# Kernel optimization log

Measured on AMD Instinct MI355X. Metric: run time of the kernel, lower is better.

The kernel has to match this reference:

```python
import jax, jax.numpy as jnp
import numpy as np

N_NODES = 100000
N_EDGES = 1600000
D_IN = 128
D_HID = 128
N_CLASSES = 8


def setup_inputs() -> dict:
    key = jax.random.key(0)
    ks = jax.random.split(key, 8)
    x = jax.random.normal(ks[0], (N_NODES, D_IN), dtype=jnp.float32)
    edge_index = jax.random.randint(ks[1], (2, N_EDGES), 0, N_NODES, dtype=jnp.int32)
    # Glorot-ish init for weights, zeros for biases (PyG GCNConv default)
    W1 = jax.random.normal(ks[2], (D_IN, D_HID), dtype=jnp.float32) / np.sqrt(D_IN)
    b1 = jnp.zeros((D_HID,), dtype=jnp.float32)
    W2 = jax.random.normal(ks[3], (D_HID, D_HID), dtype=jnp.float32) / np.sqrt(D_HID)
    b2 = jnp.zeros((D_HID,), dtype=jnp.float32)
    Wout = jax.random.normal(ks[4], (D_HID, N_CLASSES), dtype=jnp.float32) / np.sqrt(D_HID)
    bout = jnp.zeros((N_CLASSES,), dtype=jnp.float32)
    return {"x": x, "edge_index": edge_index, "W1": W1, "b1": b1,
            "W2": W2, "b2": b2, "Wout": Wout, "bout": bout}


def _gcn_conv(h, src, dst, norm, W, b, n_nodes):
    # h: [N, d_in]; src/dst: [E+N] (with self-loops); norm: [E+N]
    h = h @ W                                   # [N, d_out]
    msg = h[src] * norm[:, None]                # gather + edge-wise scale
    agg = jax.ops.segment_sum(msg, dst, num_segments=n_nodes)  # scatter-add
    return agg + b


def reference(x, edge_index, W1, b1, W2, b2, Wout, bout):
    n = x.shape[0]
    loops = jnp.arange(n, dtype=edge_index.dtype)
    src = jnp.concatenate([edge_index[0], loops])   # [E+N]
    dst = jnp.concatenate([edge_index[1], loops])   # [E+N]
    # symmetric normalization D^-1/2 (A+I) D^-1/2
    deg = jax.ops.segment_sum(jnp.ones_like(src, dtype=x.dtype), dst, num_segments=n)
    dinv = jnp.where(deg > 0, jax.lax.rsqrt(deg), 0.0)
    norm = dinv[src] * dinv[dst]                    # [E+N]

    h = _gcn_conv(x, src, dst, norm, W1, b1, n)
    h = jax.nn.relu(h)  # dropout is identity in eval mode
    h = _gcn_conv(h, src, dst, norm, W2, b2, n)
    h = jax.nn.relu(h)
    return jax.nn.softmax(h @ Wout + bout, axis=1)  # [N, 8]
```

## Files before the change

### kernel.cpp

```cpp
#include <hip/hip_runtime.h>
#include <hip/hip_fp16.h>

#define NN 100000
#define NE 1600000
#define D 128
#define NC 8
#define NBUCK 391
#define BCAP 6144
#define CHUNK 4096

typedef _Float16 half8 __attribute__((ext_vector_type(8)));
typedef float f32x4 __attribute__((ext_vector_type(4)));

__global__ __launch_bounds__(256) void k_bscatter(const int* __restrict__ src,
                                                  const int* __restrict__ dst,
                                                  int* __restrict__ bcursor,
                                                  int* __restrict__ staged, int E) {
    __shared__ int h[NBUCK];
    __shared__ int cur[NBUCK];
    const int t = threadIdx.x;
    for (int i = t; i < NBUCK; i += 256) h[i] = 0;
    __syncthreads();
    const int base0 = blockIdx.x * CHUNK;
    int4 d4[4], s4[4];
    bool val[4];
#pragma unroll
    for (int i = 0; i < 4; ++i) {
        int e = base0 + i * 1024 + t * 4;
        val[i] = e < E;
        if (val[i]) {
            d4[i] = *(const int4*)&dst[e];
            s4[i] = *(const int4*)&src[e];
            atomicAdd(&h[d4[i].x >> 8], 1);
            atomicAdd(&h[d4[i].y >> 8], 1);
            atomicAdd(&h[d4[i].z >> 8], 1);
            atomicAdd(&h[d4[i].w >> 8], 1);
        }
    }
    __syncthreads();
    for (int i = t; i < NBUCK; i += 256) {
        int c = h[i];
        cur[i] = c ? (i * BCAP + atomicAdd(&bcursor[i], c)) : 0;
    }
    __syncthreads();
#pragma unroll
    for (int i = 0; i < 4; ++i) {
        if (val[i]) {
            int p;
            p = atomicAdd(&cur[d4[i].x >> 8], 1); staged[p] = s4[i].x * 256 + (d4[i].x & 255);
            p = atomicAdd(&cur[d4[i].y >> 8], 1); staged[p] = s4[i].y * 256 + (d4[i].y & 255);
            p = atomicAdd(&cur[d4[i].z >> 8], 1); staged[p] = s4[i].z * 256 + (d4[i].z & 255);
            p = atomicAdd(&cur[d4[i].w >> 8], 1); staged[p] = s4[i].w * 256 + (d4[i].w & 255);
        }
    }
}

__global__ __launch_bounds__(256) void k_bfill(const int* __restrict__ staged,
                                               const int* __restrict__ bcursor,
                                               int* __restrict__ rowstart,
                                               int* __restrict__ cnt,
                                               float* __restrict__ dinv,
                                               int* __restrict__ csr,
                                               const float* __restrict__ W1,
                                               __half* __restrict__ wt1,
                                               const float* __restrict__ W2,
                                               __half* __restrict__ wt2) {
    const int b = blockIdx.x;
    const int t = threadIdx.x;
    if (b >= NBUCK) {
        const float* W = (b - NBUCK) ? W2 : W1;
        __half* wt = (b - NBUCK) ? wt2 : wt1;
        for (int i = t; i < D * D; i += 256) {
            int k = i >> 7, c = i & 127;
            wt[c * D + k] = __float2half(W[i]);
        }
        return;
    }
    const int bs = b * BCAP;
    const int be = bs + bcursor[b];
    __shared__ int lc[256];
    __shared__ int ls[256];
    __shared__ int sd[256];
    lc[t] = 0;
    __syncthreads();
    for (int i = bs + t; i < be; i += 256) {
        atomicAdd(&lc[staged[i] & 255], 1);
    }
    __syncthreads();
    int v = lc[t];
    sd[t] = v;
    __syncthreads();
    for (int off = 1; off < 256; off <<= 1) {
        int y = (t >= off) ? sd[t - off] : 0;
        __syncthreads();
        sd[t] += y;
        __syncthreads();
    }
    int ex = sd[t] - v;
    ls[t] = bs + ex;
    int node = (b << 8) + t;
    if (node < NN) {
        rowstart[node] = bs + ex;
        cnt[node] = v;
        dinv[node] = rsqrtf((float)(v + 1));
    }
    lc[t] = 0;
    __syncthreads();
    for (int i = bs + t; i < be; i += 256) {
        int e = staged[i];
        int li = e & 255;
        int p = atomicAdd(&lc[li], 1);
        csr[ls[li] + p] = e >> 8;
    }
}

template <bool F32IN>
__global__ __launch_bounds__(256) void k_mgemm(const void* __restrict__ Ain,
                                               const __half* __restrict__ wt,
                                               const float* __restrict__ dinv,
                                               __half* __restrict__ hout) {
    const int tid = threadIdx.x;
    const int lane = tid & 63;
    const int wave = tid >> 6;
    const int wr = wave >> 1, wc = wave & 1;
    const int row0 = blockIdx.x * 32 + wr * 16;
    const int arow = row0 + (lane & 15);
    const int kg = lane >> 4;

    half8 afrag[4];
    if constexpr (F32IN) {
        const float* A = (const float*)Ain;
#pragma unroll
        for (int s = 0; s < 4; ++s) {
            const float* p = &A[(size_t)arow * D + s * 32 + kg * 8];
            float4 f0 = *(const float4*)p;
            float4 f1 = *(const float4*)(p + 4);
            half8 a;
            a[0] = (_Float16)f0.x; a[1] = (_Float16)f0.y;
            a[2] = (_Float16)f0.z; a[3] = (_Float16)f0.w;
            a[4] = (_Float16)f1.x; a[5] = (_Float16)f1.y;
            a[6] = (_Float16)f1.z; a[7] = (_Float16)f1.w;
            afrag[s] = a;
        }
    } else {
        const __half* A = (const __half*)Ain;
#pragma unroll
        for (int s = 0; s < 4; ++s)
            afrag[s] = *(const half8*)&A[(size_t)arow * D + s * 32 + kg * 8];
    }

    f32x4 acc[4] = {};
    const int colbase = wc * 64;
#pragma unroll
    for (int c = 0; c < 4; ++c) {
        const int col = colbase + c * 16 + (lane & 15);
#pragma unroll
        for (int s = 0; s < 4; ++s) {
            half8 b = *(const half8*)&wt[col * D + s * 32 + kg * 8];
            acc[c] = __builtin_amdgcn_mfma_f32_16x16x32_f16(afrag[s], b, acc[c], 0, 0, 0);
        }
    }

#pragma unroll
    for (int r = 0; r < 4; ++r) {
        const int row = row0 + kg * 4 + r;
        const float dv = dinv[row];
#pragma unroll
        for (int c = 0; c < 4; ++c) {
            const int col = colbase + c * 16 + (lane & 15);
            hout[(size_t)row * D + col] = __float2half(acc[c][r] * dv);
        }
    }
}

__device__ inline void add8h(float* acc, float4 raw) {
    const __half2* hp = (const __half2*)&raw;
#pragma unroll
    for (int q = 0; q < 4; ++q) {
        float2 f = __half22float2(hp[q]);
        acc[2 * q] += f.x;
        acc[2 * q + 1] += f.y;
    }
}

__global__ __launch_bounds__(256) void k_agg(const __half* __restrict__ hs,
                                             const int* __restrict__ rowstart,
                                             const int* __restrict__ cnt,
                                             const int* __restrict__ csr_src,
                                             const float* __restrict__ dinv,
                                             const float* __restrict__ bias,
                                             __half* __restrict__ hout) {
    const int node = blockIdx.x * 4 + (threadIdx.x >> 6);
    const int lane = threadIdx.x & 63;
    const int g = lane >> 4;
    const int f8 = (lane & 15) << 3;

    float acc[8] = {};
    if (g == 0) add8h(acc, *(const float4*)&hs[(size_t)node * D + f8]);

    const int c = cnt[node];
    const int* __restrict__ cl = csr_src + rowstart[node];

    int t = g;
    while (t < c) {
        float4 v[8];
#pragma unroll
        for (int i = 0; i < 8; ++i) {
            int tt = t + 4 * i;
            if (tt < c) {
                int s = cl[tt];
                v[i] = *(const float4*)&hs[(size_t)s * D + f8];
            }
        }
#pragma unroll
        for (int i = 0; i < 8; ++i) {
            int tt = t + 4 * i;
            if (tt < c) add8h(acc, v[i]);
        }
        t += 32;
    }

#pragma unroll
    for (int q = 0; q < 8; ++q) {
        acc[q] += __shfl_xor(acc[q], 16);
        acc[q] += __shfl_xor(acc[q], 32);
    }

    if (g == 0) {
        const float dv = dinv[node];
        float r[8];
#pragma unroll
        for (int q = 0; q < 8; ++q) r[q] = fmaxf(fmaf(dv, acc[q], bias[f8 + q]), 0.f);
        union { float4 f; __half2 h[4]; } u;
#pragma unroll
        for (int q = 0; q < 4; ++q) u.h[q] = __floats2half2_rn(r[2 * q], r[2 * q + 1]);
        *(float4*)&hout[(size_t)node * D + f8] = u.f;
    }
}

__global__ void k_out(const __half* __restrict__ h, const float* __restrict__ Wout,
                      const float* __restrict__ bout, float* __restrict__ out, int n) {
    __shared__ float ws[D * NC];
    int tid = threadIdx.x;
    for (int i = tid; i < D * NC; i += 256) ws[i] = Wout[i];
    __syncthreads();
    int node = blockIdx.x * 32 + (tid >> 3);
    int c = tid & 7;
    if (node >= n) return;
    float acc = bout[c];
    const __half* hrow = &h[(size_t)node * D];
#pragma unroll
    for (int k8 = 0; k8 < 16; ++k8) {
        float4 raw = *(const float4*)&hrow[k8 * 8];
        const __half2* hp = (const __half2*)&raw;
#pragma unroll
        for (int q = 0; q < 4; ++q) {
            float2 f = __half22float2(hp[q]);
            int k = k8 * 8 + 2 * q;
            acc += f.x * ws[k * NC + c] + f.y * ws[(k + 1) * NC + c];
        }
    }
    float m = acc;
#pragma unroll
    for (int off = 1; off < 8; off <<= 1) m = fmaxf(m, __shfl_xor(m, off));
    float e = __expf(acc - m);
    float ssum = e;
#pragma unroll
    for (int off = 1; off < 8; off <<= 1) ssum += __shfl_xor(ssum, off);
    out[(size_t)node * NC + c] = e / ssum;
}

extern "C" void kernel_launch(void* const* d_in, const int* in_sizes, int n_in,
                              void* d_out, int out_size, void* d_ws, size_t ws_size,
                              hipStream_t stream) {
    const float* x    = (const float*)d_in[0];
    const int*   ei   = (const int*)d_in[1];
    const float* W1   = (const float*)d_in[2];
    const float* b1   = (const float*)d_in[3];
    const float* W2   = (const float*)d_in[4];
    const float* b2   = (const float*)d_in[5];
    const float* Wout = (const float*)d_in[6];
    const float* bout = (const float*)d_in[7];
    float* out = (float*)d_out;

    size_t off = 0;
    char* base = (char*)d_ws;
    auto alloc = [&](size_t bytes) -> void* {
        void* p = base + off;
        off += (bytes + 255) & ~(size_t)255;
        return p;
    };
    int*    cnt      = (int*)alloc((size_t)NN * 4);
    int*    rowstart = (int*)alloc((size_t)NN * 4);
    int*    bcursor  = (int*)alloc((size_t)(NBUCK + 1) * 4);
    int*    csr      = (int*)alloc((size_t)NBUCK * BCAP * 4);
    float*  dinv     = (float*)alloc((size_t)NN * 4);
    __half* wt1      = (__half*)alloc((size_t)D * D * 2);
    __half* wt2      = (__half*)alloc((size_t)D * D * 2);
    __half* h16a     = (__half*)alloc((size_t)NN * D * 2);
    __half* h16f     = (__half*)alloc((size_t)NN * D * 2);
    __half* h16b     = (__half*)alloc((size_t)NN * D * 2);
    int*    staged   = (int*)alloc((size_t)NBUCK * BCAP * 4);
    if (off > ws_size) return;

    const int* src = ei;
    const int* dst = ei + NE;

    int bin_grid = (NE + CHUNK - 1) / CHUNK;
    hipMemsetAsync(bcursor, 0, (size_t)NBUCK * 4, stream);
    k_bscatter<<<bin_grid, 256, 0, stream>>>(src, dst, bcursor, staged, NE);
    k_bfill<<<NBUCK + 2, 256, 0, stream>>>(staged, bcursor, rowstart, cnt, dinv, csr,
                                           W1, wt1, W2, wt2);

    int gemm_grid = NN / 32;
    int agg_grid = NN / 4;
    k_mgemm<true><<<gemm_grid, 256, 0, stream>>>(x, wt1, dinv, h16a);
    k_agg<<<agg_grid, 256, 0, stream>>>(h16a, rowstart, cnt, csr, dinv, b1, h16f);
    k_mgemm<false><<<gemm_grid, 256, 0, stream>>>(h16f, wt2, dinv, h16a);
    k_agg<<<agg_grid, 256, 0, stream>>>(h16a, rowstart, cnt, csr, dinv, b2, h16b);
    k_out<<<(NN + 31) / 32, 256, 0, stream>>>(h16b, Wout, bout, out, NN);
}
```

Before: 267.1 us.

## Compute degrees with global atomics and co-schedule bucket scatter with first GEMM

Degree counts now come from a separate pass that uses global atomics on dst, so dinv can be recomputed inline from cnt and the dinv buffer is dropped. The bucket-scatter blocks and the first-layer GEMM blocks are merged into one launch, letting the edge binning overlap the dense GEMM. The scatter chunk size is raised to four times the edge count per block. The cost is an extra pass over dst with contended global atomics, plus re-reading dst in the scatter instead of keeping it in registers.

Result: slower. 325.1 us (+21.7%).

```diff
diff --git a/kernel.cpp b/kernel.cpp
--- a/kernel.cpp
+++ b/kernel.cpp
@@ -7,123 +7,48 @@
 #define NC 8
 #define NBUCK 391
 #define BCAP 6144
-#define CHUNK 4096
+#define CHUNK 16384
+#define NBLK_SC ((NE + CHUNK - 1) / CHUNK)
 
 typedef _Float16 half8 __attribute__((ext_vector_type(8)));
 typedef float f32x4 __attribute__((ext_vector_type(4)));
 
-__global__ __launch_bounds__(256) void k_bscatter(const int* __restrict__ src,
-                                                  const int* __restrict__ dst,
-                                                  int* __restrict__ bcursor,
-                                                  int* __restrict__ staged, int E) {
-    __shared__ int h[NBUCK];
-    __shared__ int cur[NBUCK];
+__global__ __launch_bounds__(256) void k_prep(const float* __restrict__ W1,
+                                              __half* __restrict__ wt1,
+                                              const float* __restrict__ W2,
+                                              __half* __restrict__ wt2,
+                                              const int* __restrict__ dst,
+                                              int* __restrict__ cnt, int E) {
     const int t = threadIdx.x;
-    for (int i = t; i < NBUCK; i += 256) h[i] = 0;
-    __syncthreads();
-    const int base0 = blockIdx.x * CHUNK;
-    int4 d4[4], s4[4];
-    bool val[4];
-#pragma unroll
-    for (int i = 0; i < 4; ++i) {
-        int e = base0 + i * 1024 + t * 4;
-        val[i] = e < E;
-        if (val[i]) {
-            d4[i] = *(const int4*)&dst[e];
-            s4[i] = *(const int4*)&src[e];
-            atomicAdd(&h[d4[i].x >> 8], 1);
-            atomicAdd(&h[d4[i].y >> 8], 1);
-            atomicAdd(&h[d4[i].z >> 8], 1);
-            atomicAdd(&h[d4[i].w >> 8], 1);
-        }
-    }
-    __syncthreads();
-    for (int i = t; i < NBUCK; i += 256) {
-        int c = h[i];
-        cur[i] = c ? (i * BCAP + atomicAdd(&bcursor[i], c)) : 0;
-    }
-    __syncthreads();
-#pragma unroll
-    for (int i = 0; i < 4; ++i) {
-        if (val[i]) {
-            int p;
-            p = atomicAdd(&cur[d4[i].x >> 8], 1); staged[p] = s4[i].x * 256 + (d4[i].x & 255);
-            p = atomicAdd(&cur[d4[i].y >> 8], 1); staged[p] = s4[i].y * 256 + (d4[i].y & 255);
-            p = atomicAdd(&cur[d4[i].z >> 8], 1); staged[p] = s4[i].z * 256 + (d4[i].z & 255);
-            p = atomicAdd(&cur[d4[i].w >> 8], 1); staged[p] = s4[i].w * 256 + (d4[i].w & 255);
-        }
-    }
-}
-
-__global__ __launch_bounds__(256) void k_bfill(const int* __restrict__ staged,
-                                               const int* __restrict__ bcursor,
-                                               int* __restrict__ rowstart,
-                                               int* __restrict__ cnt,
-                                               float* __restrict__ dinv,
-                                               int* __restrict__ csr,
-                                               const float* __restrict__ W1,
-                                               __half* __restrict__ wt1,
-                                               const float* __restrict__ W2,
-                                               __half* __restrict__ wt2) {
-    const int b = blockIdx.x;
-    const int t = threadIdx.x;
-    if (b >= NBUCK) {
-        const float* W = (b - NBUCK) ? W2 : W1;
-        __half* wt = (b - NBUCK) ? wt2 : wt1;
+    if (blockIdx.x < 2) {
+        const float* W = blockIdx.x ? W2 : W1;
+        __half* wt = blockIdx.x ? wt2 : wt1;
         for (int i = t; i < D * D; i += 256) {
             int k = i >> 7, c = i & 127;
             wt[c * D + k] = __float2half(W[i]);
         }
         return;
     }
-    const int bs = b * BCAP;
-    const int be = bs + bcursor[b];
-    __shared__ int lc[256];
-    __shared__ int ls[256];
-    __shared__ int sd[256];
-    lc[t] = 0;
-    __syncthreads();
-    for (int i = bs + t; i < be; i += 256) {
-        atomicAdd(&lc[staged[i] & 255], 1);
-    }
-    __syncthreads();
-    int v = lc[t];
-    sd[t] = v;
-    __syncthreads();
-    for (int off = 1; off < 256; off <<= 1) {
-        int y = (t >= off) ? sd[t - off] : 0;
-        __syncthreads();
-        sd[t] += y;
-        __syncthreads();
-    }
-    int ex = sd[t] - v;
-    ls[t] = bs + ex;
-    int node = (b << 8) + t;
-    if (node < NN) {
-        rowstart[node] = bs + ex;
-        cnt[node] = v;
-        dinv[node] = rsqrtf((float)(v + 1));
-    }
-    lc[t] = 0;
-    __syncthreads();
-    for (int i = bs + t; i < be; i += 256) {
-        int e = staged[i];
-        int li = e & 255;
-        int p = atomicAdd(&lc[li], 1);
-        csr[ls[li] + p] = e >> 8;
+    int e0 = (blockIdx.x - 2) * 1024 + t * 4;
+    if (e0 < E) {
+        int4 d4 = *(const int4*)&dst[e0];
+        atomicAdd(&cnt[d4.x], 1);
+        atomicAdd(&cnt[d4.y], 1);
+        atomicAdd(&cnt[d4.z], 1);
+        atomicAdd(&cnt[d4.w], 1);
     }
 }
 
 template <bool F32IN>
-__global__ __launch_bounds__(256) void k_mgemm(const void* __restrict__ Ain,
-                                               const __half* __restrict__ wt,
-                                               const float* __restrict__ dinv,
-                                               __half* __restrict__ hout) {
+__device__ __forceinline__ void gemm_body(const void* __restrict__ Ain,
+                                          const __half* __restrict__ wt,
+                                          const int* __restrict__ cnt,
+                                          __half* __restrict__ hout, int gb) {
     const int tid = threadIdx.x;
     const int lane = tid & 63;
     const int wave = tid >> 6;
     const int wr = wave >> 1, wc = wave & 1;
-    const int row0 = blockIdx.x * 32 + wr * 16;
+    const int row0 = gb * 32 + wr * 16;
     const int arow = row0 + (lane & 15);
     const int kg = lane >> 4;
 
@@ -164,13 +89,105 @@
 #pragma unroll
     for (int r = 0; r < 4; ++r) {
         const int row = row0 + kg * 4 + r;
-        const float dv = dinv[row];
+        const float dv = rsqrtf((float)(cnt[row] + 1));
 #pragma unroll
         for (int c = 0; c < 4; ++c) {
             const int col = colbase + c * 16 + (lane & 15);
             hout[(size_t)row * D + col] = __float2half(acc[c][r] * dv);
         }
     }
+}
+
+__global__ __launch_bounds__(256) void k_work(const int* __restrict__ src,
+                                              const int* __restrict__ dst,
+                                              int* __restrict__ bcursor,
+                                              int* __restrict__ staged,
+                                              const float* __restrict__ x,
+                                              const __half* __restrict__ wt1,
+                                              const int* __restrict__ cnt,
+                                              __half* __restrict__ hout, int E) {
+    if (blockIdx.x < NBLK_SC) {
+        __shared__ int h[NBUCK];
+        __shared__ int cur[NBUCK];
+        const int t = threadIdx.x;
+        for (int i = t; i < NBUCK; i += 256) h[i] = 0;
+        __syncthreads();
+        const int base0 = blockIdx.x * CHUNK;
+#pragma unroll
+        for (int i = 0; i < CHUNK / 1024; ++i) {
+            int e = base0 + i * 1024 + t * 4;
+            if (e < E) {
+                int4 d4 = *(const int4*)&dst[e];
+                atomicAdd(&h[d4.x >> 8], 1);
+                atomicAdd(&h[d4.y >> 8], 1);
+                atomicAdd(&h[d4.z >> 8], 1);
+                atomicAdd(&h[d4.w >> 8], 1);
+            }
+        }
+        __syncthreads();
+        for (int i = t; i < NBUCK; i += 256) {
+            int c = h[i];
+            cur[i] = c ? (i * BCAP + atomicAdd(&bcursor[i], c)) : 0;
+        }
+        __syncthreads();
+#pragma unroll
+        for (int i = 0; i < CHUNK / 1024; ++i) {
+            int e = base0 + i * 1024 + t * 4;
+            if (e < E) {
+                int4 d4 = *(const int4*)&dst[e];
+                int4 s4 = *(const int4*)&src[e];
+                int p;
+                p = atomicAdd(&cur[d4.x >> 8], 1); staged[p] = s4.x * 256 + (d4.x & 255);
+                p = atomicAdd(&cur[d4.y >> 8], 1); staged[p] = s4.y * 256 + (d4.y & 255);
+                p = atomicAdd(&cur[d4.z >> 8], 1); staged[p] = s4.z * 256 + (d4.z & 255);
+                p = atomicAdd(&cur[d4.w >> 8], 1); staged[p] = s4.w * 256 + (d4.w & 255);
+            }
+        }
+        return;
+    }
+    gemm_body<true>(x, wt1, cnt, hout, blockIdx.x - NBLK_SC);
+}
+
+__global__ __launch_bounds__(256) void k_bfill(const int* __restrict__ staged,
+                                               const int* __restrict__ bcursor,
+                                               const int* __restrict__ cnt,
+                                               int* __restrict__ rowstart,
+                                               int* __restrict__ csr) {
+    const int b = blockIdx.x;
+    const int t = threadIdx.x;
+    const int bs = b * BCAP;
+    const int be = bs + bcursor[b];
+    __shared__ int ls[256];
+    __shared__ int sd[256];
+    __shared__ int lc[256];
+    const int node = (b << 8) + t;
+    int v = (node < NN) ? cnt[node] : 0;
+    sd[t] = v;
+    __syncthreads();
+    for (int off = 1; off < 256; off <<= 1) {
+        int y = (t >= off) ? sd[t - off] : 0;
+        __syncthreads();
+        sd[t] += y;
+        __syncthreads();
+    }
+    int ex = sd[t] - v;
+    ls[t] = bs + ex;
+    if (node < NN) rowstart[node] = bs + ex;
+    lc[t] = 0;
+    __syncthreads();
+    for (int i = bs + t; i < be; i += 256) {
+        int e = staged[i];
+        int li = e & 255;
+        int p = atomicAdd(&lc[li], 1);
+        csr[ls[li] + p] = e >> 8;
+    }
+}
+
+__global__ __launch_bounds__(256) void k_gemm2(const __half* __restrict__ A,
+                                               const __half* __restrict__ wt,
+                                               const int* __restrict__ cnt,
+                                               __half* __restrict__ hout) {
+    gemm_body<false>(A, wt, cnt, hout, blockIdx.x);
 }
 
 __device__ inline void add8h(float* acc, float4 raw) {
@@ -187,7 +204,6 @@
                                              const int* __restrict__ rowstart,
                                              const int* __restrict__ cnt,
                                              const int* __restrict__ csr_src,
-                                             const float* __restrict__ dinv,
                                              const float* __restrict__ bias,
                                              __half* __restrict__ hout) {
     const int node = blockIdx.x * 4 + (threadIdx.x >> 6);
@@ -227,7 +243,7 @@
     }
 
     if (g == 0) {
-        const float dv = dinv[node];
+        const float dv = rsqrtf((float)(c + 1));
         float r[8];
 #pragma unroll
         for (int q = 0; q < 8; ++q) r[q] = fmaxf(fmaf(dv, acc[q], bias[f8 + q]), 0.f);
@@ -291,10 +307,9 @@
         return p;
     };
     int*    cnt      = (int*)alloc((size_t)NN * 4);
+    int*    bcursor  = (int*)alloc((size_t)NBUCK * 4);
     int*    rowstart = (int*)alloc((size_t)NN * 4);
-    int*    bcursor  = (int*)alloc((size_t)(NBUCK + 1) * 4);
     int*    csr      = (int*)alloc((size_t)NBUCK * BCAP * 4);
-    float*  dinv     = (float*)alloc((size_t)NN * 4);
     __half* wt1      = (__half*)alloc((size_t)D * D * 2);
     __half* wt2      = (__half*)alloc((size_t)D * D * 2);
     __half* h16a     = (__half*)alloc((size_t)NN * D * 2);
@@ -306,17 +321,19 @@
     const int* src = ei;
     const int* dst = ei + NE;
 
-    int bin_grid = (NE + CHUNK - 1) / CHUNK;
-    hipMemsetAsync(bcursor, 0, (size_t)NBUCK * 4, stream);
-    k_bscatter<<<bin_grid, 256, 0, stream>>>(src, dst, bcursor, staged, NE);
-    k_bfill<<<NBUCK + 2, 256, 0, stream>>>(staged, bcursor, rowstart, cnt, dinv, csr,
-                                           W1, wt1, W2, wt2);
-
-    int gemm_grid = NN / 32;
+    hipMemsetAsync(cnt, 0, ((size_t)NN * 4 + 255 & ~(size_t)255) + (size_t)NBUCK * 4,
+                   stream);
+
+    k_prep<<<2 + (NE / 4 + 255) / 256, 256, 0, stream>>>(W1, wt1, W2, wt2, dst, cnt, NE);
+
+    k_work<<<NBLK_SC + NN / 32, 256, 0, stream>>>(src, dst, bcursor, staged,
+                                                  x, wt1, cnt, h16a, NE);
+
+    k_bfill<<<NBUCK, 256, 0, stream>>>(staged, bcursor, cnt, rowstart, csr);
+
     int agg_grid = NN / 4;
-    k_mgemm<true><<<gemm_grid, 256, 0, stream>>>(x, wt1, dinv, h16a);
-    k_agg<<<agg_grid, 256, 0, stream>>>(h16a, rowstart, cnt, csr, dinv, b1, h16f);
-    k_mgemm<false><<<gemm_grid, 256, 0, stream>>>(h16f, wt2, dinv, h16a);
-    k_agg<<<agg_grid, 256, 0, stream>>>(h16a, rowstart, cnt, csr, dinv, b2, h16b);
+    k_agg<<<agg_grid, 256, 0, stream>>>(h16a, rowstart, cnt, csr, b1, h16f);
+    k_gemm2<<<NN / 32, 256, 0, stream>>>(h16f, wt2, cnt, h16a);
+    k_agg<<<agg_grid, 256, 0, stream>>>(h16a, rowstart, cnt, csr, b2, h16b);
     k_out<<<(NN + 31) / 32, 256, 0, stream>>>(h16b, Wout, bout, out, NN);
 }
```

## Fuse first GEMM into CSR fill kernel with unscaled output and source-side scaling

Applied to the files above, without the earlier changes.

The weight transpose moves into the scatter kernel, and the first GEMM moves into the CSR-fill kernel as extra blocks, so one launch and one dependency are removed. Since dinv is not yet available when those GEMM blocks run, the first GEMM writes unscaled features. The first aggregation then multiplies each gathered neighbour row by dinv[src], which adds a per-edge scalar gather. This trades a kernel boundary for extra random loads of dinv in the layer-one aggregation.

After: 269.9 us. Within noise of the previous version (+1.1%).

```diff
diff --git a/kernel.cpp b/kernel.cpp
--- a/kernel.cpp
+++ b/kernel.cpp
@@ -8,17 +8,31 @@
 #define NBUCK 391
 #define BCAP 6144
 #define CHUNK 4096
+#define NBLK_SC ((NE + CHUNK - 1) / CHUNK)
 
 typedef _Float16 half8 __attribute__((ext_vector_type(8)));
 typedef float f32x4 __attribute__((ext_vector_type(4)));
 
-__global__ __launch_bounds__(256) void k_bscatter(const int* __restrict__ src,
-                                                  const int* __restrict__ dst,
-                                                  int* __restrict__ bcursor,
-                                                  int* __restrict__ staged, int E) {
+__global__ __launch_bounds__(256) void k_scat(const int* __restrict__ src,
+                                              const int* __restrict__ dst,
+                                              int* __restrict__ bcursor,
+                                              int* __restrict__ staged,
+                                              const float* __restrict__ W1,
+                                              __half* __restrict__ wt1,
+                                              const float* __restrict__ W2,
+                                              __half* __restrict__ wt2, int E) {
+    const int t = threadIdx.x;
+    if (blockIdx.x >= NBLK_SC) {
+        const float* W = (blockIdx.x - NBLK_SC) ? W2 : W1;
+        __half* wt = (blockIdx.x - NBLK_SC) ? wt2 : wt1;
+        for (int i = t; i < D * D; i += 256) {
+            int k = i >> 7, c = i & 127;
+            wt[c * D + k] = __float2half(W[i]);
+        }
+        return;
+    }
     __shared__ int h[NBUCK];
     __shared__ int cur[NBUCK];
-    const int t = threadIdx.x;
     for (int i = t; i < NBUCK; i += 256) h[i] = 0;
     __syncthreads();
     const int base0 = blockIdx.x * CHUNK;
@@ -55,75 +69,16 @@
     }
 }
 
-__global__ __launch_bounds__(256) void k_bfill(const int* __restrict__ staged,
-                                               const int* __restrict__ bcursor,
-                                               int* __restrict__ rowstart,
-                                               int* __restrict__ cnt,
-                                               float* __restrict__ dinv,
-                                               int* __restrict__ csr,
-                                               const float* __restrict__ W1,
-                                               __half* __restrict__ wt1,
-                                               const float* __restrict__ W2,
-                                               __half* __restrict__ wt2) {
-    const int b = blockIdx.x;
-    const int t = threadIdx.x;
-    if (b >= NBUCK) {
-        const float* W = (b - NBUCK) ? W2 : W1;
-        __half* wt = (b - NBUCK) ? wt2 : wt1;
-        for (int i = t; i < D * D; i += 256) {
-            int k = i >> 7, c = i & 127;
-            wt[c * D + k] = __float2half(W[i]);
-        }
-        return;
-    }
-    const int bs = b * BCAP;
-    const int be = bs + bcursor[b];
-    __shared__ int lc[256];
-    __shared__ int ls[256];
-    __shared__ int sd[256];
-    lc[t] = 0;
-    __syncthreads();
-    for (int i = bs + t; i < be; i += 256) {
-        atomicAdd(&lc[staged[i] & 255], 1);
-    }
-    __syncthreads();
-    int v = lc[t];
-    sd[t] = v;
-    __syncthreads();
-    for (int off = 1; off < 256; off <<= 1) {
-        int y = (t >= off) ? sd[t - off] : 0;
-        __syncthreads();
-        sd[t] += y;
-        __syncthreads();
-    }
-    int ex = sd[t] - v;
-    ls[t] = bs + ex;
-    int node = (b << 8) + t;
-    if (node < NN) {
-        rowstart[node] = bs + ex;
-        cnt[node] = v;
-        dinv[node] = rsqrtf((float)(v + 1));
-    }
-    lc[t] = 0;
-    __syncthreads();
-    for (int i = bs + t; i < be; i += 256) {
-        int e = staged[i];
-        int li = e & 255;
-        int p = atomicAdd(&lc[li], 1);
-        csr[ls[li] + p] = e >> 8;
-    }
-}
-
-template <bool F32IN>
-__global__ __launch_bounds__(256) void k_mgemm(const void* __restrict__ Ain,
-                                               const __half* __restrict__ wt,
-                                               const float* __restrict__ dinv,
-                                               __half* __restrict__ hout) {
+template <bool F32IN, bool SCALE>
+__device__ __forceinline__ void gemm_body(const void* __restrict__ Ain,
+                                          const __half* __restrict__ wt,
+                                          const float* __restrict__ dinv,
+                                          __half* __restrict__ hout, int gb) {
     const int tid = threadIdx.x;
     const int lane = tid & 63;
     const int wave = tid >> 6;
     const int wr = wave >> 1, wc = wave & 1;
-    const int row0 = blockIdx.x * 32 + wr * 16;
+    const int row0 = gb * 32 + wr * 16;
     const int arow = row0 + (lane & 15);
     const int kg = lane >> 4;
 
@@ -164,13 +119,74 @@
 #pragma unroll
     for (int r = 0; r < 4; ++r) {
         const int row = row0 + kg * 4 + r;
-        const float dv = dinv[row];
+        float dv = 1.0f;
+        if constexpr (SCALE) dv = dinv[row];
 #pragma unroll
         for (int c = 0; c < 4; ++c) {
             const int col = colbase + c * 16 + (lane & 15);
-            hout[(size_t)row * D + col] = __float2half(acc[c][r] * dv);
-        }
-    }
+            hout[(size_t)row * D + col] = __float2half(SCALE ? acc[c][r] * dv : acc[c][r]);
+        }
+    }
+}
+
+__global__ __launch_bounds__(256) void k_fg(const int* __restrict__ staged,
+                                            const int* __restrict__ bcursor,
+                                            int* __restrict__ rowstart,
+                                            int* __restrict__ cnt,
+                                            float* __restrict__ dinv,
+                                            int* __restrict__ csr,
+                                            const float* __restrict__ x,
+                                            const __half* __restrict__ wt1,
+                                            __half* __restrict__ hout) {
+    const int b = blockIdx.x;
+    if (b >= NBUCK) {
+        gemm_body<true, false>(x, wt1, nullptr, hout, b - NBUCK);
+        return;
+    }
+    const int t = threadIdx.x;
+    const int bs = b * BCAP;
+    const int be = bs + bcursor[b];
+    __shared__ int lc[256];
+    __shared__ int ls[256];
+    __shared__ int sd[256];
+    lc[t] = 0;
+    __syncthreads();
+    for (int i = bs + t; i < be; i += 256) {
+        atomicAdd(&lc[staged[i] & 255], 1);
+    }
+    __syncthreads();
+    int v = lc[t];
+    sd[t] = v;
+    __syncthreads();
+    for (int off = 1; off < 256; off <<= 1) {
+        int y = (t >= off) ? sd[t - off] : 0;
+        __syncthreads();
+        sd[t] += y;
+        __syncthreads();
+    }
+    int ex = sd[t] - v;
+    ls[t] = bs + ex;
+    int node = (b << 8) + t;
+    if (node < NN) {
+        rowstart[node] = bs + ex;
+        cnt[node] = v;
+        dinv[node] = rsqrtf((float)(v + 1));
+    }
+    lc[t] = 0;
+    __syncthreads();
+    for (int i = bs + t; i < be; i += 256) {
+        int e = staged[i];
+        int li = e & 255;
+        int p = atomicAdd(&lc[li], 1);
+        csr[ls[li] + p] = e >> 8;
+    }
+}
+
+__global__ __launch_bounds__(256) void k_gemm2(const __half* __restrict__ A,
+                                               const __half* __restrict__ wt,
+                                               const float* __restrict__ dinv,
+                                               __half* __restrict__ hout) {
+    gemm_body<false, true>(A, wt, dinv, hout, blockIdx.x);
 }
 
 __device__ inline void add8h(float* acc, float4 raw) {
@@ -183,13 +199,80 @@
     }
 }
 
-__global__ __launch_bounds__(256) void k_agg(const __half* __restrict__ hs,
-                                             const int* __restrict__ rowstart,
-                                             const int* __restrict__ cnt,
-                                             const int* __restrict__ csr_src,
-                                             const float* __restrict__ dinv,
-                                             const float* __restrict__ bias,
-                                             __half* __restrict__ hout) {
+__device__ inline void fma8h(float* acc, float4 raw, float s) {
+    const __half2* hp = (const __half2*)&raw;
+#pragma unroll
+    for (int q = 0; q < 4; ++q) {
+        float2 f = __half22float2(hp[q]);
+        acc[2 * q] = fmaf(s, f.x, acc[2 * q]);
+        acc[2 * q + 1] = fmaf(s, f.y, acc[2 * q + 1]);
+    }
+}
+
+__global__ __launch_bounds__(256) void k_agg_u(const __half* __restrict__ hs,
+                                               const int* __restrict__ rowstart,
+                                               const int* __restrict__ cnt,
+                                               const int* __restrict__ csr_src,
+                                               const float* __restrict__ dinv,
+                                               const float* __restrict__ bias,
+                                               __half* __restrict__ hout) {
+    const int node = blockIdx.x * 4 + (threadIdx.x >> 6);
+    const int lane = threadIdx.x & 63;
+    const int g = lane >> 4;
+    const int f8 = (lane & 15) << 3;
+
+    const float dvn = dinv[node];
+    float acc[8] = {};
+    if (g == 0) fma8h(acc, *(const float4*)&hs[(size_t)node * D + f8], dvn);
+
+    const int c = cnt[node];
+    const int* __restrict__ cl = csr_src + rowstart[node];
+
+    int t = g;
+    while (t < c) {
+        float4 v[8];
+        float dv8[8];
+#pragma unroll
+        for (int i = 0; i < 8; ++i) {
+            int tt = t + 4 * i;
+            if (tt < c) {
+                int s = cl[tt];
+                v[i] = *(const float4*)&hs[(size_t)s * D + f8];
+                dv8[i] = dinv[s];
+            }
+        }
+#pragma unroll
+        for (int i = 0; i < 8; ++i) {
+            int tt = t + 4 * i;
+            if (tt < c) fma8h(acc, v[i], dv8[i]);
+        }
+        t += 32;
+    }
+
+#pragma unroll
+    for (int q = 0; q < 8; ++q) {
+        acc[q] += __shfl_xor(acc[q], 16);
+        acc[q] += __shfl_xor(acc[q], 32);
+    }
+
+    if (g == 0) {
+        float r[8];
+#pragma unroll
+        for (int q = 0; q < 8; ++q) r[q] = fmaxf(fmaf(dvn, acc[q], bias[f8 + q]), 0.f);
+        union { float4 f; __half2 h[4]; } u;
+#pragma unroll
+        for (int q = 0; q < 4; ++q) u.h[q] = __floats2half2_rn(r[2 * q], r[2 * q + 1]);
+        *(float4*)&hout[(size_t)node * D + f8] = u.f;
+    }
+}
+
+__global__ __launch_bounds__(256) void k_agg_s(const __half* __restrict__ hs,
+                                               const int* __restrict__ rowstart,
+                                               const int* __restrict__ cnt,
+                                               const int* __restrict__ csr_src,
+                                               const float* __restrict__ dinv,
+                                               const float* __restrict__ bias,
+                                               __half* __restrict__ hout) {
     const int node = blockIdx.x * 4 + (threadIdx.x >> 6);
     const int lane = threadIdx.x & 63;
     const int g = lane >> 4;
@@ -292,7 +375,7 @@
     };
     int*    cnt      = (int*)alloc((size_t)NN * 4);
     int*    rowstart = (int*)alloc((size_t)NN * 4);
-    int*    bcursor  = (int*)alloc((size_t)(NBUCK + 1) * 4);
+    int*    bcursor  = (int*)alloc((size_t)NBUCK * 4);
     int*    csr      = (int*)alloc((size_t)NBUCK * BCAP * 4);
     float*  dinv     = (float*)alloc((size_t)NN * 4);
     __half* wt1      = (__half*)alloc((size_t)D * D * 2);
@@ -306,17 +389,17 @@
     const int* src = ei;
     const int* dst = ei + NE;
 
-    int bin_grid = (NE + CHUNK - 1) / CHUNK;
     hipMemsetAsync(bcursor, 0, (size_t)NBUCK * 4, stream);
-    k_bscatter<<<bin_grid, 256, 0, stream>>>(src, dst, bcursor, staged, NE);
-    k_bfill<<<NBUCK + 2, 256, 0, stream>>>(staged, bcursor, rowstart, cnt, dinv, csr,
-                                           W1, wt1, W2, wt2);
-
-    int gemm_grid = NN / 32;
+
+    k_scat<<<NBLK_SC + 2, 256, 0, stream>>>(src, dst, bcursor, staged,
+                                            W1, wt1, W2, wt2, NE);
+
+    k_fg<<<NBUCK + NN / 32, 256, 0, stream>>>(staged, bcursor, rowstart, cnt, dinv,
+                                              csr, x, wt1, h16a);
+
     int agg_grid = NN / 4;
-    k_mgemm<true><<<gemm_grid, 256, 0, stream>>>(x, wt1, dinv, h16a);
-    k_agg<<<agg_grid, 256, 0, stream>>>(h16a, rowstart, cnt, csr, dinv, b1, h16f);
-    k_mgemm<false><<<gemm_grid, 256, 0, stream>>>(h16f, wt2, dinv, h16a);
-    k_agg<<<agg_grid, 256, 0, stream>>>(h16a, rowstart, cnt, csr, dinv, b2, h16b);
+    k_agg_u<<<agg_grid, 256, 0, stream>>>(h16a, rowstart, cnt, csr, dinv, b1, h16f);
+    k_gemm2<<<NN / 32, 256, 0, stream>>>(h16f, wt2, dinv, h16a);
+    k_agg_s<<<agg_grid, 256, 0, stream>>>(h16a, rowstart, cnt, csr, dinv, b2, h16b);
     k_out<<<(NN + 31) / 32, 256, 0, stream>>>(h16b, Wout, bout, out, NN);
 }
```

## Coarsen CSR build buckets to 2048 nodes and move weight conversion into scatter

Applied to the files above, without the earlier changes.

The destination-bucketed CSR construction now uses 49 buckets of 2048 nodes each instead of 391 buckets of 256. Each scatter block therefore appends longer runs per bucket and issues fewer global cursor atomics, and the fill kernel gains an 8-per-thread local prefix scan. The fp16 weight-transpose work moves from the fill kernel into extra blocks of the scatter kernel. The cost is that the fill stage runs only 49 blocks, each handling about 32K edges, which leaves most of the GPU idle during that phase.

Result: slower. 321.9 us (+20.5%).

```diff
diff --git a/kernel.cpp b/kernel.cpp
--- a/kernel.cpp
+++ b/kernel.cpp
@@ -5,21 +5,36 @@
 #define NE 1600000
 #define D 128
 #define NC 8
-#define NBUCK 391
-#define BCAP 6144
+#define BNODES 2048
+#define NBUCK 49
+#define BCAP 36864
 #define CHUNK 4096
+#define NBLK_SC ((NE + CHUNK - 1) / CHUNK)
 
 typedef _Float16 half8 __attribute__((ext_vector_type(8)));
 typedef float f32x4 __attribute__((ext_vector_type(4)));
 
-__global__ __launch_bounds__(256) void k_bscatter(const int* __restrict__ src,
-                                                  const int* __restrict__ dst,
-                                                  int* __restrict__ bcursor,
-                                                  int* __restrict__ staged, int E) {
+__global__ __launch_bounds__(256) void k_scat(const int* __restrict__ src,
+                                              const int* __restrict__ dst,
+                                              int* __restrict__ bcursor,
+                                              int* __restrict__ staged,
+                                              const float* __restrict__ W1,
+                                              __half* __restrict__ wt1,
+                                              const float* __restrict__ W2,
+                                              __half* __restrict__ wt2, int E) {
+    const int t = threadIdx.x;
+    if (blockIdx.x >= NBLK_SC) {
+        const float* W = (blockIdx.x - NBLK_SC) ? W2 : W1;
+        __half* wt = (blockIdx.x - NBLK_SC) ? wt2 : wt1;
+        for (int i = t; i < D * D; i += 256) {
+            int k = i >> 7, c = i & 127;
+            wt[c * D + k] = __float2half(W[i]);
+        }
+        return;
+    }
     __shared__ int h[NBUCK];
     __shared__ int cur[NBUCK];
-    const int t = threadIdx.x;
-    for (int i = t; i < NBUCK; i += 256) h[i] = 0;
+    if (t < NBUCK) h[t] = 0;
     __syncthreads();
     const int base0 = blockIdx.x * CHUNK;
     int4 d4[4], s4[4];
@@ -31,26 +46,26 @@
         if (val[i]) {
             d4[i] = *(const int4*)&dst[e];
             s4[i] = *(const int4*)&src[e];
-            atomicAdd(&h[d4[i].x >> 8], 1);
-            atomicAdd(&h[d4[i].y >> 8], 1);
-            atomicAdd(&h[d4[i].z >> 8], 1);
-            atomicAdd(&h[d4[i].w >> 8], 1);
-        }
-    }
-    __syncthreads();
-    for (int i = t; i < NBUCK; i += 256) {
-        int c = h[i];
-        cur[i] = c ? (i * BCAP + atomicAdd(&bcursor[i], c)) : 0;
+            atomicAdd(&h[d4[i].x >> 11], 1);
+            atomicAdd(&h[d4[i].y >> 11], 1);
+            atomicAdd(&h[d4[i].z >> 11], 1);
+            atomicAdd(&h[d4[i].w >> 11], 1);
+        }
+    }
+    __syncthreads();
+    if (t < NBUCK) {
+        int c = h[t];
+        cur[t] = c ? (t * BCAP + atomicAdd(&bcursor[t], c)) : 0;
     }
     __syncthreads();
 #pragma unroll
     for (int i = 0; i < 4; ++i) {
         if (val[i]) {
             int p;
-            p = atomicAdd(&cur[d4[i].x >> 8], 1); staged[p] = s4[i].x * 256 + (d4[i].x & 255);
-            p = atomicAdd(&cur[d4[i].y >> 8], 1); staged[p] = s4[i].y * 256 + (d4[i].y & 255);
-            p = atomicAdd(&cur[d4[i].z >> 8], 1); staged[p] = s4[i].z * 256 + (d4[i].z & 255);
-            p = atomicAdd(&cur[d4[i].w >> 8], 1); staged[p] = s4[i].w * 256 + (d4[i].w & 255);
+            p = atomicAdd(&cur[d4[i].x >> 11], 1); staged[p] = (s4[i].x << 11) | (d4[i].x & 2047);
+            p = atomicAdd(&cur[d4[i].y >> 11], 1); staged[p] = (s4[i].y << 11) | (d4[i].y & 2047);
+            p = atomicAdd(&cur[d4[i].z >> 11], 1); staged[p] = (s4[i].z << 11) | (d4[i].z & 2047);
+            p = atomicAdd(&cur[d4[i].w >> 11], 1); staged[p] = (s4[i].w << 11) | (d4[i].w & 2047);
         }
     }
 }
@@ -60,35 +75,25 @@
                                                int* __restrict__ rowstart,
                                                int* __restrict__ cnt,
                                                float* __restrict__ dinv,
-                                               int* __restrict__ csr,
-                                               const float* __restrict__ W1,
-                                               __half* __restrict__ wt1,
-                                               const float* __restrict__ W2,
-                                               __half* __restrict__ wt2) {
+                                               int* __restrict__ csr) {
     const int b = blockIdx.x;
     const int t = threadIdx.x;
-    if (b >= NBUCK) {
-        const float* W = (b - NBUCK) ? W2 : W1;
-        __half* wt = (b - NBUCK) ? wt2 : wt1;
-        for (int i = t; i < D * D; i += 256) {
-            int k = i >> 7, c = i & 127;
-            wt[c * D + k] = __float2half(W[i]);
-        }
-        return;
-    }
     const int bs = b * BCAP;
     const int be = bs + bcursor[b];
-    __shared__ int lc[256];
-    __shared__ int ls[256];
+    __shared__ int lc[BNODES];
+    __shared__ int ls[BNODES];
     __shared__ int sd[256];
-    lc[t] = 0;
-    __syncthreads();
-    for (int i = bs + t; i < be; i += 256) {
-        atomicAdd(&lc[staged[i] & 255], 1);
-    }
-    __syncthreads();
-    int v = lc[t];
-    sd[t] = v;
+#pragma unroll
+    for (int j = 0; j < 8; ++j) lc[t + j * 256] = 0;
+    __syncthreads();
+    for (int i = bs + t; i < be; i += 256)
+        atomicAdd(&lc[staged[i] & (BNODES - 1)], 1);
+    __syncthreads();
+    int loc[8];
+    int s = 0;
+#pragma unroll
+    for (int j = 0; j < 8; ++j) { loc[j] = s; s += lc[t * 8 + j]; }
+    sd[t] = s;
     __syncthreads();
     for (int off = 1; off < 256; off <<= 1) {
         int y = (t >= off) ? sd[t - off] : 0;
@@ -96,29 +101,36 @@
         sd[t] += y;
         __syncthreads();
     }
-    int ex = sd[t] - v;
-    ls[t] = bs + ex;
-    int node = (b << 8) + t;
-    if (node < NN) {
-        rowstart[node] = bs + ex;
-        cnt[node] = v;
-        dinv[node] = rsqrtf((float)(v + 1));
-    }
-    lc[t] = 0;
+    int base = sd[t] - s;
+#pragma unroll
+    for (int j = 0; j < 8; ++j) ls[t * 8 + j] = bs + base + loc[j];
+    __syncthreads();
+    const int node0 = b * BNODES;
+    for (int idx = t; idx < BNODES; idx += 256) {
+        int node = node0 + idx;
+        if (node < NN) {
+            int c = lc[idx];
+            rowstart[node] = ls[idx];
+            cnt[node] = c;
+            dinv[node] = rsqrtf((float)(c + 1));
+        }
+    }
+#pragma unroll
+    for (int j = 0; j < 8; ++j) lc[t + j * 256] = 0;
     __syncthreads();
     for (int i = bs + t; i < be; i += 256) {
         int e = staged[i];
-        int li = e & 255;
+        int li = e & (BNODES - 1);
         int p = atomicAdd(&lc[li], 1);
-        csr[ls[li] + p] = e >> 8;
+        csr[ls[li] + p] = e >> 11;
     }
 }
 
 template <bool F32IN>
-__global__ __launch_bounds__(256) void k_mgemm(const void* __restrict__ Ain,
-                                               const __half* __restrict__ wt,
-                                               const float* __restrict__ dinv,
-                                               __half* __restrict__ hout) {
+__global__ __launch_bounds__(256) void k_gemm(const void* __restrict__ Ain,
+                                              const __half* __restrict__ wt,
+                                              const float* __restrict__ dinv,
+                                              __half* __restrict__ hout) {
     const int tid = threadIdx.x;
     const int lane = tid & 63;
     const int wave = tid >> 6;
@@ -292,7 +304,7 @@
     };
     int*    cnt      = (int*)alloc((size_t)NN * 4);
     int*    rowstart = (int*)alloc((size_t)NN * 4);
-    int*    bcursor  = (int*)alloc((size_t)(NBUCK + 1) * 4);
+    int*    bcursor  = (int*)alloc((size_t)NBUCK * 4);
     int*    csr      = (int*)alloc((size_t)NBUCK * BCAP * 4);
     float*  dinv     = (float*)alloc((size_t)NN * 4);
     __half* wt1      = (__half*)alloc((size_t)D * D * 2);
@@ -306,17 +318,17 @@
     const int* src = ei;
     const int* dst = ei + NE;
 
-    int bin_grid = (NE + CHUNK - 1) / CHUNK;
     hipMemsetAsync(bcursor, 0, (size_t)NBUCK * 4, stream);
-    k_bscatter<<<bin_grid, 256, 0, stream>>>(src, dst, bcursor, staged, NE);
-    k_bfill<<<NBUCK + 2, 256, 0, stream>>>(staged, bcursor, rowstart, cnt, dinv, csr,
-                                           W1, wt1, W2, wt2);
+
+    k_scat<<<NBLK_SC + 2, 256, 0, stream>>>(src, dst, bcursor, staged,
+                                            W1, wt1, W2, wt2, NE);
+    k_bfill<<<NBUCK, 256, 0, stream>>>(staged, bcursor, rowstart, cnt, dinv, csr);
 
     int gemm_grid = NN / 32;
     int agg_grid = NN / 4;
-    k_mgemm<true><<<gemm_grid, 256, 0, stream>>>(x, wt1, dinv, h16a);
+    k_gemm<true><<<gemm_grid, 256, 0, stream>>>(x, wt1, dinv, h16a);
     k_agg<<<agg_grid, 256, 0, stream>>>(h16a, rowstart, cnt, csr, dinv, b1, h16f);
-    k_mgemm<false><<<gemm_grid, 256, 0, stream>>>(h16f, wt2, dinv, h16a);
+    k_gemm<false><<<gemm_grid, 256, 0, stream>>>(h16f, wt2, dinv, h16a);
     k_agg<<<agg_grid, 256, 0, stream>>>(h16a, rowstart, cnt, csr, dinv, b2, h16b);
     k_out<<<(NN + 31) / 32, 256, 0, stream>>>(h16b, Wout, bout, out, NN);
 }
```
